# Optimization experiments

Measured on AMD Instinct MI355X. Metric: run time of the kernel, lower is better.

Reference implementation:

```python
import jax, jax.numpy as jnp
import numpy as np

H = 256   # hidden_size
B = 64    # batch_size
LP = 2048 # passage length
LQ = 64   # question length


def _linear(x, W, b):
    # torch nn.Linear: y = x @ W.T + b
    return jnp.matmul(x, W.T) + b


def _gru_cell(x, h, w_ih, w_hh, b_ih, b_hh):
    # torch GRUCell semantics: x is input, h is hidden state
    gi = jnp.matmul(x, w_ih.T) + b_ih   # [B, 3*2H]
    gh = jnp.matmul(h, w_hh.T) + b_hh
    i_r, i_z, i_n = jnp.split(gi, 3, axis=-1)
    h_r, h_z, h_n = jnp.split(gh, 3, axis=-1)
    r = jax.nn.sigmoid(i_r + h_r)
    z = jax.nn.sigmoid(i_z + h_z)
    n = jnp.tanh(i_n + r * h_n)
    return (1.0 - z) * n + z * h


def setup_inputs() -> dict:
    key = jax.random.key(0)
    ks = jax.random.split(key, 17)
    s = lambda i, shape: jax.random.normal(ks[i], shape, dtype=jnp.float32) * 0.05
    return {
        "passEnc": jax.random.normal(ks[0], (LP, B, 2 * H), dtype=jnp.float32),
        "quesEnc": jax.random.normal(ks[1], (LQ, B, 2 * H), dtype=jnp.float32),
        "WQu_W": s(2, (H, 2 * H)), "WQu_b": s(3, (H,)),
        "WQv_W": s(4, (H, H)),     "WQv_b": s(5, (H,)),
        "WPh_W": s(6, (H, 2 * H)), "WPh_b": s(7, (H,)),
        "Wah_W": s(8, (H, 2 * H)), "Wah_b": s(9, (H,)),
        "Vt1": s(10, (B, H, 1)),
        "Vt2": s(11, (B, H, 1)),
        "VQr": s(12, (1, 1, H)),
        "gru_wih": s(13, (6 * H, 2 * H)), "gru_whh": s(14, (6 * H, 2 * H)),
        "gru_bih": s(15, (6 * H,)),       "gru_bhh": s(16, (6 * H,)),
    }


def reference(passEnc, quesEnc, WQu_W, WQu_b, WQv_W, WQv_b, WPh_W, WPh_b,
              Wah_W, Wah_b, Vt1, Vt2, VQr, gru_wih, gru_whh, gru_bih, gru_bhh):
    # --- question-aware initial state rQ ---
    # temp: [lQ, B, H] (VQr path broadcasts over lQ and B)
    temp = jnp.tanh(_linear(quesEnc, WQu_W, WQu_b) + _linear(VQr, WQv_W, WQv_b))
    sQ = jnp.einsum('qbh,bh->bq', temp, Vt1[..., 0])          # [B, lQ]
    a = jax.nn.softmax(sQ, axis=1)
    rQ = jnp.einsum('bq,qbd->bd', a, quesEnc)                 # [B, 2H]

    passP = _linear(passEnc, WPh_W, WPh_b)                    # [lP, B, H], reused both steps

    def pointer_step(rQ):
        temp2 = jnp.tanh(passP + _linear(rQ, Wah_W, Wah_b))   # [lP, B, H]
        sP = jnp.einsum('pbh,bh->bp', temp2, Vt2[..., 0])     # [B, lP]
        aP = jax.nn.softmax(sP, axis=1)
        ct = jnp.einsum('bp,pbd->bd', aP, passEnc)            # [B, 2H]
        return aP, ct

    aP1, ct = pointer_step(rQ)
    rQ = _gru_cell(rQ, ct, gru_wih, gru_whh, gru_bih, gru_bhh)
    aP2, _ = pointer_step(rQ)
    return (aP1, aP2)


if __name__ == "__main__":
    out = reference(**setup_inputs())
    print(out[0].shape, out[1].shape)
```

## Files before the change

kernel.cpp:

```cpp
#include <hip/hip_runtime.h>
#include <math.h>


constexpr int Bn   = 64;
constexpr int Hn   = 256;
constexpr int D2H  = 512;
constexpr int LPn  = 2048;
constexpr int LQn  = 64;

typedef __attribute__((ext_vector_type(8))) short bf16x8;
typedef __attribute__((ext_vector_type(4))) float f32x4;

typedef const __attribute__((address_space(1))) unsigned int* gup;
typedef __attribute__((address_space(3))) unsigned int* lup;
__device__ inline void async16(const void* g, void* l) {
  __builtin_amdgcn_global_load_lds((gup)g, (lup)l, 16, 0, 0);
}

__device__ inline float waveAllSum(float v) {
  #pragma unroll
  for (int o = 32; o > 0; o >>= 1) v += __shfl_xor(v, o, 64);
  return v;
}
__device__ inline float waveAllMax(float v) {
  #pragma unroll
  for (int o = 32; o > 0; o >>= 1) v = fmaxf(v, __shfl_xor(v, o, 64));
  return v;
}

__device__ inline short f2bf_rtne(float f) {
  union { float f; unsigned u; } v; v.f = f;
  unsigned r = v.u + 0x7FFF + ((v.u >> 16) & 1);
  return (short)(r >> 16);
}
__device__ inline unsigned pk2(float lo, float hi) {
  union { float f; unsigned u; } a, b; a.f = lo; b.f = hi;
  return __builtin_amdgcn_perm(b.u + 0x8000u, a.u + 0x8000u, 0x07060302u);
}
__device__ inline bf16x8 cvt8(f32x4 a0, f32x4 a1) {
  union { unsigned u[4]; bf16x8 v; } r;
  r.u[0] = pk2(a0[0], a0[1]);
  r.u[1] = pk2(a0[2], a0[3]);
  r.u[2] = pk2(a1[0], a1[1]);
  r.u[3] = pk2(a1[2], a1[3]);
  return r.v;
}

__global__ __launch_bounds__(256) void k_wcvt(const float* __restrict__ WQu,
                                              const float* __restrict__ WPh,
                                              short* __restrict__ q16,
                                              short* __restrict__ p16) {
  int e = (blockIdx.x * 256 + threadIdx.x) * 4;
  const float* src; short* dst; int off;
  if (e < 131072) { src = WQu; dst = q16; off = e; }
  else            { src = WPh; dst = p16; off = e - 131072; }
  f32x4 f = *(const f32x4*)&src[off];
  short4 h;
  h.x = f2bf_rtne(f[0]); h.y = f2bf_rtne(f[1]);
  h.z = f2bf_rtne(f[2]); h.w = f2bf_rtne(f[3]);
  *(short4*)&dst[off] = h;
}

__global__ __launch_bounds__(256) void k_v2(const float* __restrict__ VQr,
                                            const float* __restrict__ WQv_W,
                                            const float* __restrict__ WQv_b,
                                            float* __restrict__ v2) {
  __shared__ float s[256];
  int t = threadIdx.x;
  s[t] = VQr[t];
  __syncthreads();
  float acc = WQv_b[t];
  for (int k = 0; k < 256; ++k) acc += s[k] * WQv_W[t * 256 + k];
  v2[t] = acc;
}

__global__ __launch_bounds__(256, 4) void k_mfma(
    const float* __restrict__ A,
    const short* __restrict__ Wb,
    const float* __restrict__ bias,
    const float* __restrict__ u,
    const float* __restrict__ vt,
    short* __restrict__ pp,
    float* __restrict__ sOut,
    int ustride, int sstride)
{
  __shared__ union {
    struct { short As[128 * 64]; short Bs[128 * 64]; } m;
    float sred[256];
  } sm;
  const int t = threadIdx.x;
  const int w = t >> 6, l = t & 63, l15 = l & 15, quad = l >> 4;
  const int wm = w >> 1, wn = w & 1;
  const long bm = (long)blockIdx.y * 128;
  const int n0 = blockIdx.x * 128;

  f32x4 acc[4][4];
  #pragma unroll
  for (int i = 0; i < 4; ++i)
    #pragma unroll
    for (int j = 0; j < 4; ++j)
      acc[i][j] = (f32x4)0.f;

  const short* gB = Wb + (size_t)(n0 + (t >> 3)) * 512 + (((t & 7) ^ ((t >> 3) & 7)) << 3);
  short* lB = sm.m.Bs + t * 8;

  for (int k0 = 0; k0 < 512; k0 += 64) {
    #pragma unroll
    for (int it = 0; it < 4; ++it)
      async16(gB + it * 16384 + k0, lB + it * 2048);
    f32x4 a0[4], a1[4];
    #pragma unroll
    for (int s = 0; s < 4; ++s) {
      const int e = s * 256 + t, row = e >> 3, c = e & 7;
      const float* g = A + (bm + row) * 512 + k0 + (c << 3);
      a0[s] = *(const f32x4*)g;
      a1[s] = *(const f32x4*)(g + 4);
    }
    #pragma unroll
    for (int s = 0; s < 4; ++s) {
      const int e = s * 256 + t, row = e >> 3, c = e & 7;
      *(bf16x8*)&sm.m.As[row * 64 + ((c ^ (row & 7)) << 3)] = cvt8(a0[s], a1[s]);
    }
    __syncthreads();
    #pragma unroll
    for (int ks = 0; ks < 2; ++ks) {
      bf16x8 af[4], bfv[4];
      const int cc = ks * 4 + quad;
      #pragma unroll
      for (int i = 0; i < 4; ++i) {
        const int R = wm * 64 + i * 16 + l15;
        af[i] = *(const bf16x8*)&sm.m.As[R * 64 + ((cc ^ (l15 & 7)) << 3)];
      }
      #pragma unroll
      for (int j = 0; j < 4; ++j) {
        const int R = wn * 64 + j * 16 + l15;
        bfv[j] = *(const bf16x8*)&sm.m.Bs[R * 64 + ((cc ^ (l15 & 7)) << 3)];
      }
      #pragma unroll
      for (int i = 0; i < 4; ++i)
        #pragma unroll
        for (int j = 0; j < 4; ++j)
          acc[i][j] = __builtin_amdgcn_mfma_f32_16x16x32_bf16(af[i], bfv[j], acc[i][j], 0, 0, 0);
    }
    __syncthreads();
  }

  short* ppt = pp ? pp + (((size_t)blockIdx.y * 2 + blockIdx.x) * 16384 + (size_t)w * 4096 + l * 8)
                  : nullptr;
  float srow[4][4];
  #pragma unroll
  for (int i = 0; i < 4; ++i) {
    #pragma unroll
    for (int r = 0; r < 4; ++r) srow[i][r] = 0.f;
    unsigned pk[8];
    const int bb = i * 16 + quad * 4;
    #pragma unroll
    for (int j = 0; j < 4; ++j) {
      const int n = n0 + wn * 64 + j * 16 + l15;
      const float bn = bias[n];
      float v0 = acc[i][j][0] + bn, v1 = acc[i][j][1] + bn;
      float v2 = acc[i][j][2] + bn, v3 = acc[i][j][3] + bn;
      if (ppt) { pk[j * 2] = pk2(v0, v1); pk[j * 2 + 1] = pk2(v2, v3); }
      srow[i][0] += tanhf(v0 + u[ustride * (bb + 0) + n]) * vt[(bb + 0) * 256 + n];
      srow[i][1] += tanhf(v1 + u[ustride * (bb + 1) + n]) * vt[(bb + 1) * 256 + n];
      srow[i][2] += tanhf(v2 + u[ustride * (bb + 2) + n]) * vt[(bb + 2) * 256 + n];
      srow[i][3] += tanhf(v3 + u[ustride * (bb + 3) + n]) * vt[(bb + 3) * 256 + n];
    }
    if (ppt) {
      uint4 s0 = {pk[0], pk[1], pk[2], pk[3]};
      uint4 s1 = {pk[4], pk[5], pk[6], pk[7]};
      *(uint4*)&ppt[i * 1024]       = s0;
      *(uint4*)&ppt[i * 1024 + 512] = s1;
    }
  }
  #pragma unroll
  for (int off = 1; off < 16; off <<= 1)
    #pragma unroll
    for (int i = 0; i < 4; ++i)
      #pragma unroll
      for (int r = 0; r < 4; ++r)
        srow[i][r] += __shfl_xor(srow[i][r], off, 64);
  if (l15 == 0)
    #pragma unroll
    for (int i = 0; i < 4; ++i)
      #pragma unroll
      for (int r = 0; r < 4; ++r)
        sm.sred[wn * 128 + wm * 64 + i * 16 + quad * 4 + r] = srow[i][r];
  __syncthreads();
  if (t < 128) {
    float s = sm.sred[t] + sm.sred[128 + t];
    int b = t & 63;
    int pg = blockIdx.y * 2 + (t >> 6);
    atomicAdd(&sOut[(size_t)b * sstride + pg], s);
  }
}

__global__ __launch_bounds__(256) void k_sp2(const short* __restrict__ pp,
                                             const float* __restrict__ u2,
                                             const float* __restrict__ vt,
                                             float* __restrict__ sP) {
  __shared__ float sred[256];
  const int g = blockIdx.x, t = threadIdx.x;
  const int w = t >> 6, l = t & 63, l15 = l & 15, quad = l >> 4;
  const int wm = w >> 1, wn = w & 1;
  const int n0 = (g & 1) * 128;
  const short* src = pp + (size_t)g * 16384 + (size_t)w * 4096 + l * 8;
  float srow[4][4];
  #pragma unroll
  for (int i = 0; i < 4; ++i) {
    uint4 q0 = *(const uint4*)&src[i * 1024];
    uint4 q1 = *(const uint4*)&src[i * 1024 + 512];
    unsigned pk[8] = {q0.x, q0.y, q0.z, q0.w, q1.x, q1.y, q1.z, q1.w};
    #pragma unroll
    for (int r = 0; r < 4; ++r) srow[i][r] = 0.f;
    const int bb = i * 16 + quad * 4;
    #pragma unroll
    for (int j = 0; j < 4; ++j) {
      const int n = n0 + wn * 64 + j * 16 + l15;
      #pragma unroll
      for (int r = 0; r < 4; ++r) {
        unsigned word = pk[j * 2 + (r >> 1)];
        unsigned bits = (r & 1) ? (word & 0xFFFF0000u) : (word << 16);
        float val = __uint_as_float(bits);
        srow[i][r] += tanhf(val + u2[(bb + r) * 256 + n]) * vt[(bb + r) * 256 + n];
      }
    }
  }
  #pragma unroll
  for (int off = 1; off < 16; off <<= 1)
    #pragma unroll
    for (int i = 0; i < 4; ++i)
      #pragma unroll
      for (int r = 0; r < 4; ++r)
        srow[i][r] += __shfl_xor(srow[i][r], off, 64);
  if (l15 == 0)
    #pragma unroll
    for (int i = 0; i < 4; ++i)
      #pragma unroll
      for (int r = 0; r < 4; ++r)
        sred[wn * 128 + wm * 64 + i * 16 + quad * 4 + r] = srow[i][r];
  __syncthreads();
  if (t < 128) {
    float s = sred[t] + sred[128 + t];
    int b = t & 63;
    int pg = (g >> 1) * 2 + (t >> 6);
    atomicAdd(&sP[(size_t)b * LPn + pg], s);
  }
}

__global__ __launch_bounds__(256) void k_rq_u1(const float* __restrict__ sQ,
                                               const float* __restrict__ quesEnc,
                                               const float* __restrict__ Wah,
                                               const float* __restrict__ Wah_b,
                                               float* __restrict__ rQ,
                                               float* __restrict__ u1) {
  int b = blockIdx.x, tid = threadIdx.x;
  __shared__ float s_a[LQn];
  __shared__ float s_r[D2H];
  if (tid < 64) {
    float s = sQ[b * LQn + tid];
    float m = waveAllMax(s);
    float e = expf(s - m);
    float sum = waveAllSum(e);
    s_a[tid] = e / sum;
  }
  __syncthreads();
  #pragma unroll
  for (int rep = 0; rep < 2; ++rep) {
    int d = tid + rep * 256;
    float acc = 0.f;
    for (int q = 0; q < LQn; ++q)
      acc += s_a[q] * quesEnc[(size_t)(q * Bn + b) * D2H + d];
    s_r[d] = acc;
    rQ[b * D2H + d] = acc;
  }
  __syncthreads();
  float accu = Wah_b[tid];
  const float* wr = Wah + (size_t)tid * 512;
  for (int k4 = 0; k4 < 128; ++k4) {
    f32x4 wv = *(const f32x4*)&wr[k4 * 4];
    f32x4 rv = *(const f32x4*)&s_r[k4 * 4];
    accu += wv[0] * rv[0] + wv[1] * rv[1] + wv[2] * rv[2] + wv[3] * rv[3];
  }
  u1[b * Hn + tid] = accu;
}

__global__ __launch_bounds__(256) void k_softmax(const float* __restrict__ sP,
                                                 float* __restrict__ out) {
  int b = blockIdx.x, tid = threadIdx.x;
  int lane = tid & 63, wid = tid >> 6;
  __shared__ float red[4];
  float v[8];
  float m = -1e30f;
  #pragma unroll
  for (int i = 0; i < 8; ++i) {
    v[i] = sP[b * LPn + i * 256 + tid];
    m = fmaxf(m, v[i]);
  }
  m = waveAllMax(m);
  if (lane == 0) red[wid] = m;
  __syncthreads();
  m = fmaxf(fmaxf(red[0], red[1]), fmaxf(red[2], red[3]));
  float s = 0.f;
  #pragma unroll
  for (int i = 0; i < 8; ++i) { v[i] = expf(v[i] - m); s += v[i]; }
  s = waveAllSum(s);
  __syncthreads();
  if (lane == 0) red[wid] = s;
  __syncthreads();
  s = red[0] + red[1] + red[2] + red[3];
  float inv = 1.0f / s;
  #pragma unroll
  for (int i = 0; i < 8; ++i) out[b * LPn + i * 256 + tid] = v[i] * inv;
}

__global__ __launch_bounds__(256) void k_ct(const float* __restrict__ aP,
                                            const float* __restrict__ passEnc,
                                            float* __restrict__ ct) {
  int b = blockIdx.x, pc = blockIdx.y, tid = threadIdx.x;
  int dg = tid & 127;
  int pg = tid >> 7;
  f32x4 acc = (f32x4)0.f;
  #pragma unroll
  for (int pp = 0; pp < 32; ++pp) {
    int p = pc * 64 + pg * 32 + pp;
    float a = aP[b * LPn + p];
    acc += a * *(const f32x4*)&passEnc[((size_t)p * Bn + b) * D2H + dg * 4];
  }
  __shared__ f32x4 sacc[256];
  sacc[tid] = acc;
  __syncthreads();
  if (pg == 0) {
    acc += sacc[tid + 128];
    float* dst = &ct[b * D2H + dg * 4];
    atomicAdd(dst + 0, acc[0]);
    atomicAdd(dst + 1, acc[1]);
    atomicAdd(dst + 2, acc[2]);
    atomicAdd(dst + 3, acc[3]);
  }
}

__global__ __launch_bounds__(256) void k_gih(const float* __restrict__ rQ,
                                             const float* __restrict__ ct,
                                             const float* __restrict__ wih,
                                             const float* __restrict__ whh,
                                             const float* __restrict__ bih,
                                             const float* __restrict__ bhh,
                                             float* __restrict__ gi,
                                             float* __restrict__ gh) {
  __shared__ float sw[16 * 512];
  int blk = blockIdx.x;
  bool isH = blk >= 96;
  const float* W = isH ? whh : wih;
  const float* X = isH ? ct : rQ;
  const float* bias = isH ? bhh : bih;
  float* G = isH ? gh : gi;
  int r0 = (isH ? blk - 96 : blk) * 16;
  int t = threadIdx.x;
  #pragma unroll
  for (int it = 0; it < 8; ++it) {
    int f4 = it * 256 + t;
    *(f32x4*)&sw[f4 * 4] = *(const f32x4*)&W[(size_t)r0 * 512 + f4 * 4];
  }
  __syncthreads();
  int b = t & 63;
  int rbase = (t >> 6) * 4;
  const float* x = X + b * 512;
  float acc[4];
  #pragma unroll
  for (int oo = 0; oo < 4; ++oo) acc[oo] = bias[r0 + rbase + oo];
  for (int k4 = 0; k4 < 128; ++k4) {
    f32x4 xv = *(const f32x4*)&x[k4 * 4];
    #pragma unroll
    for (int oo = 0; oo < 4; ++oo) {
      f32x4 wv = *(const f32x4*)&sw[(rbase + oo) * 512 + k4 * 4];
      acc[oo] += wv[0] * xv[0] + wv[1] * xv[1] + wv[2] * xv[2] + wv[3] * xv[3];
    }
  }
  #pragma unroll
  for (int oo = 0; oo < 4; ++oo)
    G[b * 1536 + r0 + rbase + oo] = acc[oo];
}

__global__ __launch_bounds__(256) void k_gates(const float* __restrict__ gi,
                                               const float* __restrict__ gh,
                                               const float* __restrict__ ct,
                                               float* __restrict__ rQ2) {
  int idx = blockIdx.x * 256 + threadIdx.x;
  int b = idx >> 9;
  int j = idx & 511;
  const float* gib = gi + b * 1536;
  const float* ghb = gh + b * 1536;
  float r = 1.f / (1.f + expf(-(gib[j] + ghb[j])));
  float z = 1.f / (1.f + expf(-(gib[512 + j] + ghb[512 + j])));
  float n = tanhf(gib[1024 + j] + r * ghb[1024 + j]);
  rQ2[b * D2H + j] = (1.f - z) * n + z * ct[b * D2H + j];
}

__global__ __launch_bounds__(256) void k_u2(const float* __restrict__ rQ2,
                                            const float* __restrict__ Wah,
                                            const float* __restrict__ Wah_b,
                                            float* __restrict__ u2) {
  int m = blockIdx.x, n = threadIdx.x;
  __shared__ float s_r[D2H];
  s_r[n]       = rQ2[m * D2H + n];
  s_r[n + 256] = rQ2[m * D2H + n + 256];
  __syncthreads();
  float acc = Wah_b[n];
  const float* wr = Wah + (size_t)n * 512;
  for (int k4 = 0; k4 < 128; ++k4) {
    f32x4 wv = *(const f32x4*)&wr[k4 * 4];
    f32x4 rv = *(const f32x4*)&s_r[k4 * 4];
    acc += wv[0] * rv[0] + wv[1] * rv[1] + wv[2] * rv[2] + wv[3] * rv[3];
  }
  u2[m * Hn + n] = acc;
}

extern "C" void kernel_launch(void* const* d_in, const int* in_sizes, int n_in,
                              void* d_out, int out_size, void* d_ws, size_t ws_size,
                              hipStream_t stream) {
  const float* passEnc  = (const float*)d_in[0];
  const float* quesEnc  = (const float*)d_in[1];
  const float* WQu_W    = (const float*)d_in[2];
  const float* WQu_b    = (const float*)d_in[3];
  const float* WQv_W    = (const float*)d_in[4];
  const float* WQv_b    = (const float*)d_in[5];
  const float* WPh_W    = (const float*)d_in[6];
  const float* WPh_b    = (const float*)d_in[7];
  const float* Wah_W    = (const float*)d_in[8];
  const float* Wah_b    = (const float*)d_in[9];
  const float* Vt1      = (const float*)d_in[10];
  const float* Vt2      = (const float*)d_in[11];
  const float* VQr      = (const float*)d_in[12];
  const float* gru_wih  = (const float*)d_in[13];
  const float* gru_whh  = (const float*)d_in[14];
  const float* gru_bih  = (const float*)d_in[15];
  const float* gru_bhh  = (const float*)d_in[16];
  float* out = (float*)d_out;

  float* ws = (float*)d_ws;
  float* v2    = ws;
  float* rQ    = v2 + 256;
  float* u1    = rQ + 32768;
  float* u2    = u1 + 16384;
  float* sP    = u2 + 16384;
  float* ct    = sP + 131072;
  float* gi    = ct + 32768;
  float* gh    = gi + 98304;
  float* rQ2   = gh + 98304;
  float* sQ    = rQ2 + 32768;
  short* wqu16 = (short*)(sQ + 4096);
  short* wph16 = wqu16 + 131072;
  short* pp16  = wph16 + 131072;

  hipMemsetAsync(sQ, 0, Bn * LQn * sizeof(float), stream);
  hipMemsetAsync(sP, 0, Bn * LPn * sizeof(float), stream);
  hipMemsetAsync(ct, 0, Bn * D2H * sizeof(float), stream);

  k_wcvt<<<256, 256, 0, stream>>>(WQu_W, WPh_W, wqu16, wph16);
  k_v2<<<1, 256, 0, stream>>>(VQr, WQv_W, WQv_b, v2);

  k_mfma<<<dim3(2, LQn * Bn / 128), 256, 0, stream>>>(
      quesEnc, wqu16, WQu_b, v2, Vt1, nullptr, sQ, 0, LQn);
  k_rq_u1<<<Bn, 256, 0, stream>>>(sQ, quesEnc, Wah_W, Wah_b, rQ, u1);

  k_mfma<<<dim3(2, LPn * Bn / 128), 256, 0, stream>>>(
      passEnc, wph16, WPh_b, u1, Vt2, pp16, sP, Hn, LPn);
  k_softmax<<<Bn, 256, 0, stream>>>(sP, out);

  k_ct<<<dim3(Bn, 32), 256, 0, stream>>>(out, passEnc, ct);

  k_gih<<<192, 256, 0, stream>>>(rQ, ct, gru_wih, gru_whh, gru_bih, gru_bhh, gi, gh);
  k_gates<<<Bn * D2H / 256, 256, 0, stream>>>(gi, gh, ct, rQ2);
  k_u2<<<Bn, 256, 0, stream>>>(rQ2, Wah_W, Wah_b, u2);

  hipMemsetAsync(sP, 0, Bn * LPn * sizeof(float), stream);
  k_sp2<<<LPn * Bn / 64, 256, 0, stream>>>(pp16, u2, Vt2, sP);
  k_softmax<<<Bn, 256, 0, stream>>>(sP, out + Bn * LPn);
}
```

Before: 922.2 us.

## Pre-convert activations to bf16 and load A tiles asynchronously into LDS

Adds a separate kernel that converts passEnc and quesEnc to bf16 up front. The GEMM kernel can then stream A tiles straight into LDS with async global-to-LDS loads instead of loading fp32 through registers and converting in the loop. It also switches to a 1D grid that assigns the two N-halves of 8 consecutive M tiles to nearby blocks, which should improve L2 reuse. The cost is an extra full pass over the large passEnc tensor (read fp32, write bf16) plus a large new workspace buffer, which may outweigh the savings in the GEMM.

```diff
diff --git a/kernel.cpp b/kernel.cpp
--- a/kernel.cpp
+++ b/kernel.cpp
@@ -61,6 +61,23 @@
   *(short4*)&dst[off] = h;
 }
 
+__global__ __launch_bounds__(256) void k_acvt(const float* __restrict__ pe,
+                                              const float* __restrict__ qe,
+                                              short* __restrict__ pe16,
+                                              short* __restrict__ qe16) {
+  const long NPG = 8388608;
+  const long NG  = 8650752;
+  for (long g = (long)blockIdx.x * 256 + threadIdx.x; g < NG;
+       g += (long)gridDim.x * 256) {
+    const float* src; short* dst; long off;
+    if (g < NPG) { src = pe; dst = pe16; off = g << 3; }
+    else         { src = qe; dst = qe16; off = (g - NPG) << 3; }
+    f32x4 a = *(const f32x4*)&src[off];
+    f32x4 b = *(const f32x4*)&src[off + 4];
+    *(bf16x8*)&dst[off] = cvt8(a, b);
+  }
+}
+
 __global__ __launch_bounds__(256) void k_v2(const float* __restrict__ VQr,
                                             const float* __restrict__ WQv_W,
                                             const float* __restrict__ WQv_b,
@@ -75,7 +92,7 @@
 }
 
 __global__ __launch_bounds__(256, 4) void k_mfma(
-    const float* __restrict__ A,
+    const short* __restrict__ Ab,
     const short* __restrict__ Wb,
     const float* __restrict__ bias,
     const float* __restrict__ u,
@@ -91,8 +108,12 @@
   const int t = threadIdx.x;
   const int w = t >> 6, l = t & 63, l15 = l & 15, quad = l >> 4;
   const int wm = w >> 1, wn = w & 1;
-  const long bm = (long)blockIdx.y * 128;
-  const int n0 = blockIdx.x * 128;
+  const int lin   = blockIdx.x;
+  const int grp   = lin >> 4;
+  const int half  = (lin & 15) >> 3;
+  const int mtile = grp * 8 + (lin & 7);
+  const long bm = (long)mtile * 128;
+  const int n0 = half * 128;
 
   f32x4 acc[4][4];
   #pragma unroll
@@ -101,26 +122,18 @@
     for (int j = 0; j < 4; ++j)
       acc[i][j] = (f32x4)0.f;
 
+  const short* gA = Ab + (size_t)(bm + (t >> 3)) * 512 + (((t & 7) ^ ((t >> 3) & 7)) << 3);
   const short* gB = Wb + (size_t)(n0 + (t >> 3)) * 512 + (((t & 7) ^ ((t >> 3) & 7)) << 3);
+  short* lA = sm.m.As + t * 8;
   short* lB = sm.m.Bs + t * 8;
 
   for (int k0 = 0; k0 < 512; k0 += 64) {
+    #pragma unroll
+    for (int it = 0; it < 4; ++it)
+      async16(gA + it * 16384 + k0, lA + it * 2048);
     #pragma unroll
     for (int it = 0; it < 4; ++it)
       async16(gB + it * 16384 + k0, lB + it * 2048);
-    f32x4 a0[4], a1[4];
-    #pragma unroll
-    for (int s = 0; s < 4; ++s) {
-      const int e = s * 256 + t, row = e >> 3, c = e & 7;
-      const float* g = A + (bm + row) * 512 + k0 + (c << 3);
-      a0[s] = *(const f32x4*)g;
-      a1[s] = *(const f32x4*)(g + 4);
-    }
-    #pragma unroll
-    for (int s = 0; s < 4; ++s) {
-      const int e = s * 256 + t, row = e >> 3, c = e & 7;
-      *(bf16x8*)&sm.m.As[row * 64 + ((c ^ (row & 7)) << 3)] = cvt8(a0[s], a1[s]);
-    }
     __syncthreads();
     #pragma unroll
     for (int ks = 0; ks < 2; ++ks) {
@@ -145,7 +158,7 @@
     __syncthreads();
   }
 
-  short* ppt = pp ? pp + (((size_t)blockIdx.y * 2 + blockIdx.x) * 16384 + (size_t)w * 4096 + l * 8)
+  short* ppt = pp ? pp + (((size_t)mtile * 2 + half) * 16384 + (size_t)w * 4096 + l * 8)
                   : nullptr;
   float srow[4][4];
   #pragma unroll
@@ -190,7 +203,7 @@
   if (t < 128) {
     float s = sm.sred[t] + sm.sred[128 + t];
     int b = t & 63;
-    int pg = blockIdx.y * 2 + (t >> 6);
+    int pg = mtile * 2 + (t >> 6);
     atomicAdd(&sOut[(size_t)b * sstride + pg], s);
   }
 }
@@ -452,20 +465,23 @@
   short* wqu16 = (short*)(sQ + 4096);
   short* wph16 = wqu16 + 131072;
   short* pp16  = wph16 + 131072;
+  short* pe16  = pp16 + 33554432;
+  short* qe16  = pe16 + 67108864;
 
   hipMemsetAsync(sQ, 0, Bn * LQn * sizeof(float), stream);
   hipMemsetAsync(sP, 0, Bn * LPn * sizeof(float), stream);
   hipMemsetAsync(ct, 0, Bn * D2H * sizeof(float), stream);
 
   k_wcvt<<<256, 256, 0, stream>>>(WQu_W, WPh_W, wqu16, wph16);
+  k_acvt<<<2048, 256, 0, stream>>>(passEnc, quesEnc, pe16, qe16);
   k_v2<<<1, 256, 0, stream>>>(VQr, WQv_W, WQv_b, v2);
 
-  k_mfma<<<dim3(2, LQn * Bn / 128), 256, 0, stream>>>(
-      quesEnc, wqu16, WQu_b, v2, Vt1, nullptr, sQ, 0, LQn);
+  k_mfma<<<LQn * Bn / 64, 256, 0, stream>>>(
+      qe16, wqu16, WQu_b, v2, Vt1, nullptr, sQ, 0, LQn);
   k_rq_u1<<<Bn, 256, 0, stream>>>(sQ, quesEnc, Wah_W, Wah_b, rQ, u1);
 
-  k_mfma<<<dim3(2, LPn * Bn / 128), 256, 0, stream>>>(
-      passEnc, wph16, WPh_b, u1, Vt2, pp16, sP, Hn, LPn);
+  k_mfma<<<LPn * Bn / 64, 256, 0, stream>>>(
+      pe16, wph16, WPh_b, u1, Vt2, pp16, sP, Hn, LPn);
   k_softmax<<<Bn, 256, 0, stream>>>(sP, out);
 
   k_ct<<<dim3(Bn, 32), 256, 0, stream>>>(out, passEnc, ct);
```

Result: faster. 902.3 us (-2.2%).

## Load fp32 A tiles asynchronously into LDS and remap grid for L2 reuse

Applied to the files above, without the earlier changes.

The MFMA GEMM kernel now streams the fp32 A tile straight into LDS with global_load_lds in an MFMA-fragment-friendly layout, and converts to bf16 at fragment-read time instead of loading through registers and converting before the LDS store. The B tile layout is rearranged to match direct per-lane fragment reads, and the grid is linearised so the two N-halves of groups of 8 M-tiles are scheduled close together, improving L2 reuse of the A rows. LDS use doubles (fp32 A), so the launch bound drops to 3 blocks per CU. The conversion cost moves into the inner loop, where it is repeated per wave.

```diff
diff --git a/kernel.cpp b/kernel.cpp
--- a/kernel.cpp
+++ b/kernel.cpp
@@ -74,7 +74,7 @@
   v2[t] = acc;
 }
 
-__global__ __launch_bounds__(256, 4) void k_mfma(
+__global__ __launch_bounds__(256, 3) void k_mfma(
     const float* __restrict__ A,
     const short* __restrict__ Wb,
     const float* __restrict__ bias,
@@ -85,14 +85,18 @@
     int ustride, int sstride)
 {
   __shared__ union {
-    struct { short As[128 * 64]; short Bs[128 * 64]; } m;
+    struct { float As[32 * 256]; short Bs[16 * 512]; } m;
     float sred[256];
   } sm;
   const int t = threadIdx.x;
   const int w = t >> 6, l = t & 63, l15 = l & 15, quad = l >> 4;
   const int wm = w >> 1, wn = w & 1;
-  const long bm = (long)blockIdx.y * 128;
-  const int n0 = blockIdx.x * 128;
+  const int lin   = blockIdx.x;
+  const int grp   = lin >> 4;
+  const int half  = (lin & 15) >> 3;
+  const int mtile = grp * 8 + (lin & 7);
+  const long bm = (long)mtile * 128;
+  const int n0 = half * 128;
 
   f32x4 acc[4][4];
   #pragma unroll
@@ -101,40 +105,36 @@
     for (int j = 0; j < 4; ++j)
       acc[i][j] = (f32x4)0.f;
 
-  const short* gB = Wb + (size_t)(n0 + (t >> 3)) * 512 + (((t & 7) ^ ((t >> 3) & 7)) << 3);
-  short* lB = sm.m.Bs + t * 8;
+  const int fcA = ((t >> 7) << 3) | (((t >> 4) & 3) << 1) | ((t >> 6) & 1);
+  const float* gA = A + (bm + (t & 15)) * 512 + fcA * 4;
+  const int cB = (((t >> 6) & 1) << 2) | ((t >> 4) & 3);
+  const short* gB = Wb + (size_t)(n0 + ((t >> 7) << 4) + (t & 15)) * 512 + cB * 8;
+  char* lA = (char*)sm.m.As + t * 16;
+  char* lB = (char*)sm.m.Bs + t * 16;
 
   for (int k0 = 0; k0 < 512; k0 += 64) {
     #pragma unroll
+    for (int it = 0; it < 8; ++it)
+      async16(gA + it * 8192 + k0, lA + it * 4096);
+    #pragma unroll
     for (int it = 0; it < 4; ++it)
-      async16(gB + it * 16384 + k0, lB + it * 2048);
-    f32x4 a0[4], a1[4];
-    #pragma unroll
-    for (int s = 0; s < 4; ++s) {
-      const int e = s * 256 + t, row = e >> 3, c = e & 7;
-      const float* g = A + (bm + row) * 512 + k0 + (c << 3);
-      a0[s] = *(const f32x4*)g;
-      a1[s] = *(const f32x4*)(g + 4);
-    }
-    #pragma unroll
-    for (int s = 0; s < 4; ++s) {
-      const int e = s * 256 + t, row = e >> 3, c = e & 7;
-      *(bf16x8*)&sm.m.As[row * 64 + ((c ^ (row & 7)) << 3)] = cvt8(a0[s], a1[s]);
-    }
+      async16(gB + it * 16384 + k0, lB + it * 4096);
     __syncthreads();
+    const int lb = l * 4;
     #pragma unroll
     for (int ks = 0; ks < 2; ++ks) {
       bf16x8 af[4], bfv[4];
-      const int cc = ks * 4 + quad;
       #pragma unroll
       for (int i = 0; i < 4; ++i) {
-        const int R = wm * 64 + i * 16 + l15;
-        af[i] = *(const bf16x8*)&sm.m.As[R * 64 + ((cc ^ (l15 & 7)) << 3)];
+        const int pl = ((wm * 4 + i) * 4 + ks * 2) * 256;
+        f32x4 p0 = *(const f32x4*)&sm.m.As[pl + lb];
+        f32x4 p1 = *(const f32x4*)&sm.m.As[pl + 256 + lb];
+        af[i] = cvt8(p0, p1);
       }
       #pragma unroll
       for (int j = 0; j < 4; ++j) {
-        const int R = wn * 64 + j * 16 + l15;
-        bfv[j] = *(const bf16x8*)&sm.m.Bs[R * 64 + ((cc ^ (l15 & 7)) << 3)];
+        const int rg = ((wn * 4 + j) * 2 + ks) * 512;
+        bfv[j] = *(const bf16x8*)&sm.m.Bs[rg + l * 8];
       }
       #pragma unroll
       for (int i = 0; i < 4; ++i)
@@ -145,7 +145,7 @@
     __syncthreads();
   }
 
-  short* ppt = pp ? pp + (((size_t)blockIdx.y * 2 + blockIdx.x) * 16384 + (size_t)w * 4096 + l * 8)
+  short* ppt = pp ? pp + (((size_t)mtile * 2 + half) * 16384 + (size_t)w * 4096 + l * 8)
                   : nullptr;
   float srow[4][4];
   #pragma unroll
@@ -190,7 +190,7 @@
   if (t < 128) {
     float s = sm.sred[t] + sm.sred[128 + t];
     int b = t & 63;
-    int pg = blockIdx.y * 2 + (t >> 6);
+    int pg = mtile * 2 + (t >> 6);
     atomicAdd(&sOut[(size_t)b * sstride + pg], s);
   }
 }
@@ -460,11 +460,11 @@
   k_wcvt<<<256, 256, 0, stream>>>(WQu_W, WPh_W, wqu16, wph16);
   k_v2<<<1, 256, 0, stream>>>(VQr, WQv_W, WQv_b, v2);
 
-  k_mfma<<<dim3(2, LQn * Bn / 128), 256, 0, stream>>>(
+  k_mfma<<<LQn * Bn / 64, 256, 0, stream>>>(
       quesEnc, wqu16, WQu_b, v2, Vt1, nullptr, sQ, 0, LQn);
   k_rq_u1<<<Bn, 256, 0, stream>>>(sQ, quesEnc, Wah_W, Wah_b, rQ, u1);
 
-  k_mfma<<<dim3(2, LPn * Bn / 128), 256, 0, stream>>>(
+  k_mfma<<<LPn * Bn / 64, 256, 0, stream>>>(
       passEnc, wph16, WPh_b, u1, Vt2, pp16, sP, Hn, LPn);
   k_softmax<<<Bn, 256, 0, stream>>>(sP, out);
 
```

After: 832.3 us. -9.8%, faster.
